# Optimization experiments

Measured on AMD Instinct MI355X. Metric: run time of the kernel, lower is better.

The kernel has to match this reference:

```python
import jax, jax.numpy as jnp
from jax import lax
import numpy as np

# (in_ch, out_ch, kernel) per SparseConv layer; last layer has no ReLU
LAYERS = [(1, 16, 11), (16, 16, 7), (16, 16, 5), (16, 16, 3), (16, 16, 3), (16, 1, 1)]
DN = ('NCHW', 'OIHW', 'NCHW')


def _sparse_conv(x, mask, w, bias, gamma, beta, relu):
    k = w.shape[-1]
    p = k // 2
    pad = [(p, p), (p, p)]
    xm = x * mask  # mask broadcasts over channels ([B,1,H,W])
    y = lax.conv_general_dilated(xm, w, (1, 1), pad, dimension_numbers=DN)
    # 'sparsity' conv: fixed all-ones [1,1,k,k] kernel over the 1-channel mask
    ones_k = jnp.ones((1, 1, k, k), x.dtype)
    s = lax.conv_general_dilated(mask, ones_k, (1, 1), pad, dimension_numbers=DN)
    y = y * (1.0 / (s + 1e-8)) + bias[None, :, None, None]
    # BatchNorm2d in training mode (batch statistics), eps=1e-5
    mean = jnp.mean(y, axis=(0, 2, 3), keepdims=True)
    var = jnp.var(y, axis=(0, 2, 3), keepdims=True)
    y = (y - mean) * lax.rsqrt(var + 1e-5)
    y = y * gamma[None, :, None, None] + beta[None, :, None, None]
    if relu:
        y = jnp.maximum(y, 0.0)
    # MaxPool2d(k, stride=1, padding=k//2) on the mask (pads with -inf)
    mask = lax.reduce_window(mask, -jnp.inf, lax.max, (1, 1, k, k), (1, 1, 1, 1),
                             [(0, 0), (0, 0), (p, p), (p, p)])
    return y, mask


def setup_inputs() -> dict:
    key = jax.random.key(0)
    kx, *kws = jax.random.split(key, 1 + len(LAYERS))
    inp = {"x": jax.random.uniform(kx, (4, 2, 1024, 1024), dtype=jnp.float32)}
    for i, (cin, cout, k) in enumerate(LAYERS, start=1):
        fan_in = cin * k * k
        inp[f"w{i}"] = jax.random.normal(kws[i - 1], (cout, cin, k, k), jnp.float32) / np.sqrt(fan_in)
        inp[f"b{i}"] = jnp.zeros((cout,), jnp.float32)
        inp[f"g{i}"] = jnp.ones((cout,), jnp.float32)
        inp[f"bt{i}"] = jnp.zeros((cout,), jnp.float32)
    return inp


def reference(x, w1, b1, g1, bt1, w2, b2, g2, bt2, w3, b3, g3, bt3,
              w4, b4, g4, bt4, w5, b5, g5, bt5, w6, b6, g6, bt6):
    data = x[:, 0:1]   # channels != 1 (input_channels=2 -> channel 0)
    mask = x[:, 1:2]   # channel 1
    params = [(w1, b1, g1, bt1), (w2, b2, g2, bt2), (w3, b3, g3, bt3),
              (w4, b4, g4, bt4), (w5, b5, g5, bt5), (w6, b6, g6, bt6)]
    h, m = data, mask
    for i, (w, b, g, bt) in enumerate(params):
        h, m = _sparse_conv(h, m, w, b, g, bt, relu=(i < 5))
    return h
```

## Files before the change

kernel.cpp:

```cpp
#include <hip/hip_runtime.h>
#include <hip/hip_bf16.h>


#define HW (1024 * 1024)
typedef __hip_bfloat16 bf16;
typedef __attribute__((ext_vector_type(8))) short s8v;
typedef __attribute__((ext_vector_type(4))) float f4v;

__device__ __forceinline__ float b2f(bf16 v) { return __bfloat162float(v); }
__device__ __forceinline__ bf16  f2b(float v) { return __float2bfloat16(v); }
__device__ __forceinline__ short fbits(float v) {
    bf16 t = f2b(v); short s; __builtin_memcpy(&s, &t, 2); return s;
}
__device__ __forceinline__ float bs2f(short s) {
    bf16 t; __builtin_memcpy(&t, &s, 2); return __bfloat162float(t);
}

__device__ __forceinline__ float ldv(const void* p, int i, bool isf) {
    return isf ? ((const float*)p)[i] : b2f(((const bf16*)p)[i]);
}

__device__ __forceinline__ float wave_reduce(float v) {
    #pragma unroll
    for (int off = 32; off > 0; off >>= 1)
        v += __shfl_down(v, off, 64);
    return v;
}

__global__ void probeKernel(const unsigned short* __restrict__ xb,
                            float* __restrict__ stats)
{
    __shared__ int sbad;
    const int tid = threadIdx.x;
    if (tid == 0) sbad = 0;
    __syncthreads();
    int bad = 0;
    for (int i = tid; i < 4096; i += 256) {
        unsigned u = ((unsigned)xb[i]) << 16;
        float v = __uint_as_float(u);
        if (!(v >= 0.f && v < 1.f)) bad = 1;
    }
    if (bad) sbad = 1;
    __syncthreads();
    if (tid == 0) stats[380] = sbad ? 1.f : 0.f;
}

__global__ void transposeW1(const void* __restrict__ w, bf16* __restrict__ wb,
                            const float* flagp)
{
    const bool isf = (*flagp > 0.5f);
    int j = blockIdx.x * 256 + threadIdx.x;
    if (j < 3072) {
        int col8 = j & 7;
        int co = (j >> 3) & 15;
        int k8 = j >> 7;
        int k = k8 * 8 + col8;
        int dy = k >> 4, dx = k & 15;
        float v = (dy < 11 && dx < 11) ? ldv(w, co * 121 + dy * 11 + dx, isf) : 0.f;
        wb[j] = f2b(v);
    }
}

__global__ void transposeWB(const void* __restrict__ w, bf16* __restrict__ wtB,
                            int K, int DXP, const float* flagp)
{
    const bool isf = (*flagp > 0.5f);
    int NT = K * DXP;
    int j = blockIdx.x * 256 + threadIdx.x;
    if (j < NT * 256) {
        int t = j >> 8, co = (j >> 4) & 15, c = j & 15;
        int dy = t / DXP, dx = t % DXP;
        float v = (dx < K) ? ldv(w, (co * 16 + c) * (K * K) + dy * K + dx, isf) : 0.f;
        wtB[j] = f2b(v);
    }
}

template <int TM, int TK, int WP, int BS>
__device__ __forceinline__ void buildMaskTile(
    const void* __restrict__ mask0, bool isf, float* sm0, float* vm,
    float* mprev, int bx, int by, int tid)
{
    constexpr int H1 = (TM - 32) / 2;
    constexpr int H2 = (TK - 32) / 2;
    for (int i = tid; i < TM * TM; i += BS) {
        int yy = by - H1 + i / TM, xx = bx - H1 + i % TM;
        float m = 0.f;
        if ((unsigned)yy < 1024u && (unsigned)xx < 1024u)
            m = ldv(mask0, (yy << 10) + xx, isf);
        sm0[i] = m;
    }
    __syncthreads();
    for (int i = tid; i < TK * TM; i += BS) {
        int y = i / TM, xc = i % TM;
        float mx = 0.f;
        for (int d = 0; d < WP; ++d) mx = fmaxf(mx, sm0[(y + d) * TM + xc]);
        vm[i] = mx;
    }
    __syncthreads();
    for (int i = tid; i < TK * TK; i += BS) {
        int y = i / TK, xc = i % TK;
        int gy = by - H2 + y, gx = bx - H2 + xc;
        float mx = 0.f;
        if ((unsigned)gy < 1024u && (unsigned)gx < 1024u)
            for (int d = 0; d < WP; ++d) mx = fmaxf(mx, vm[y * TM + xc + d]);
        mprev[i] = mx;
    }
    __syncthreads();
}

__device__ __forceinline__ const void* maskChanPtr(const void* x, int n, bool isf) {
    return isf ? (const void*)((const float*)x + n * 2 * HW + HW)
               : (const void*)((const bf16*)x + n * 2 * HW + HW);
}

__global__ __launch_bounds__(256) void convFirstM(
    const void* __restrict__ x, const bf16* __restrict__ wb1,
    const void* __restrict__ bias, bf16* __restrict__ out,
    float* statsCur, const float* flagp)
{
    constexpr int ST = 48, ROWS = 44, MT = 42;
    __shared__ alignas(16) short c0[ROWS * ST];
    __shared__ alignas(16) short c1[ROWS * ST + 2];
    __shared__ float smask[MT * MT];
    __shared__ float scs[32 * MT];
    __shared__ float sinv[1024];
    __shared__ float red[128];
    const bool isf = (*flagp > 0.5f);
    const int n = blockIdx.z;
    const int bx = blockIdx.x * 32, by = blockIdx.y * 32;
    const int tid = threadIdx.x, lane = tid & 63, wid = tid >> 6;
    const int nn = lane & 15, q = lane >> 4;

    s8v Bf[6];
    #pragma unroll
    for (int kb = 0; kb < 6; ++kb)
        Bf[kb] = *(const s8v*)(wb1 + ((kb * 4 + q) * 16 + nn) * 8);
    const float bv = ldv(bias, nn, isf);

    if (tid == 0) c1[0] = 0;

    const int xoff = n * 2 * HW;
    for (int i = tid; i < ROWS * ST; i += 256) {
        int row = i / ST, col = i - row * ST;
        int yy = by - 5 + row, xx = bx - 5 + col;
        float d = 0.f, m = 0.f;
        if ((unsigned)yy < 1024u && (unsigned)xx < 1024u) {
            d = ldv(x, xoff + (yy << 10) + xx, isf);
            m = ldv(x, xoff + HW + (yy << 10) + xx, isf);
        }
        short b = fbits(d * m);
        c0[i] = b;
        c1[i + 1] = b;
        if (row < MT && col < MT) smask[row * MT + col] = m;
    }
    __syncthreads();

    for (int i = tid; i < 32 * MT; i += 256) {
        int r = i / MT, c = i - r * MT;
        float s = 0.f;
        #pragma unroll
        for (int dy = 0; dy < 11; ++dy) s += smask[(r + dy) * MT + c];
        scs[i] = s;
    }
    __syncthreads();
    for (int i = tid; i < 1024; i += 256) {
        int r = i >> 5, xc = i & 31;
        float s = 0.f;
        #pragma unroll
        for (int dx = 0; dx < 11; ++dx) s += scs[r * MT + xc + dx];
        sinv[i] = 121.f / (s + 1e-8f);
    }
    __syncthreads();

    const int dyq = q >> 1, dxq = (q & 1) << 3;
    const size_t nbase = (size_t)n * HW;
    float lsum = 0.f, lsq = 0.f;

    for (int mt = 0; mt < 16; ++mt) {
        int idx = wid * 16 + mt;
        int r = idx >> 1, g = idx & 1;
        int e = (r + dyq) * ST + (g << 4) + dxq + nn;
        int s = e & 1;
        const unsigned* cp = s ? (const unsigned*)c1 : (const unsigned*)c0;
        int w = (e + s) >> 1;
        f4v acc0 = {0.f, 0.f, 0.f, 0.f}, acc1 = {0.f, 0.f, 0.f, 0.f};
        #pragma unroll
        for (int kb = 0; kb < 6; ++kb) {
            union { unsigned u[4]; s8v v; } A;
            A.u[0] = cp[w];
            A.u[1] = cp[w + 1];
            A.u[2] = cp[w + 2];
            A.u[3] = cp[w + 3];
            if (kb & 1)
                acc1 = __builtin_amdgcn_mfma_f32_16x16x32_bf16(A.v, Bf[kb], acc1, 0, 0, 0);
            else
                acc0 = __builtin_amdgcn_mfma_f32_16x16x32_bf16(A.v, Bf[kb], acc0, 0, 0, 0);
            w += ST;
        }
        #pragma unroll
        for (int i2 = 0; i2 < 4; ++i2) {
            int px = (g << 4) + (q << 2) + i2;
            float y = fmaf(acc0[i2] + acc1[i2], sinv[(r << 5) + px], bv);
            out[((nbase + ((by + r) << 10) + bx + px) << 4) + nn] = f2b(y);
            lsum += y;
            lsq = fmaf(y, y, lsq);
        }
    }

    lsum += __shfl_xor(lsum, 16, 64);
    lsum += __shfl_xor(lsum, 32, 64);
    lsq  += __shfl_xor(lsq, 16, 64);
    lsq  += __shfl_xor(lsq, 32, 64);
    if (lane < 16) {
        red[wid * 32 + lane]      = lsum;
        red[wid * 32 + 16 + lane] = lsq;
    }
    __syncthreads();
    if (tid < 32) {
        float t = red[tid] + red[32 + tid] + red[64 + tid] + red[96 + tid];
        atomicAdd(&statsCur[tid], t);
    }
}

template <int K, int WP, int DXP, int JG>
__global__ __launch_bounds__(512, 4) void conv16m(
    const bf16* __restrict__ in, const void* __restrict__ x,
    const bf16* __restrict__ wtB, const float* statsPrev,
    const void* __restrict__ bias, bf16* __restrict__ out,
    float* statsCur, const float* flagp)
{
    constexpr int TK = 32 + K - 1;
    constexpr int TM = TK + WP - 1;
    constexpr int NJ = DXP / 2;
    constexpr int NJG = NJ / JG;
    static_assert(NJ % JG == 0, "NJ must be divisible by JG");
    constexpr int KK = K * K;
    constexpr int H2 = K / 2;
    __shared__ short sdatL[(TK * TK + 1) * 8];
    __shared__ short sdatH[(TK * TK + 1) * 8];
    __shared__ float mprev[TK * TK];
    __shared__ float sinv[1024];
    __shared__ float red[256];
    __shared__ float sss[32];
    const bool isf = (*flagp > 0.5f);
    const int n = blockIdx.z;
    const int bx = blockIdx.x * 32, by = blockIdx.y * 32;
    const int tid = threadIdx.x, lane = tid & 63, wid = tid >> 6;

    if (tid < 16) { sss[tid] = statsPrev[32 + tid]; sss[16 + tid] = statsPrev[48 + tid]; }

    buildMaskTile<TM, TK, WP, 512>(maskChanPtr(x, n, isf), isf,
                                   (float*)sdatL, (float*)sdatH, mprev, bx, by, tid);

    {
        float* cs = (float*)sdatH;
        for (int i = tid; i < 32 * TK; i += 512) {
            int r = i / TK, c = i - r * TK;
            float s = 0.f;
            #pragma unroll
            for (int dy = 0; dy < K; ++dy) s += mprev[(r + dy) * TK + c];
            cs[i] = s;
        }
        __syncthreads();
        for (int i = tid; i < 1024; i += 512) {
            int r = i >> 5, xc = i & 31;
            float s = 0.f;
            #pragma unroll
            for (int dx = 0; dx < K; ++dx) s += cs[r * TK + xc + dx];
            sinv[i] = (float)KK / (s + 1e-8f);
        }
        __syncthreads();
    }

    const int nn = lane & 15, quad = lane >> 4, c0 = (quad & 1) * 8, tl = quad >> 1;

    {
        const bf16* inb = in + ((size_t)n * HW << 4);
        for (int p = tid; p < TK * TK; p += 512) {
            int yy = by - H2 + p / TK, xx = bx - H2 + p % TK;
            s8v lo = {0,0,0,0,0,0,0,0}, hi = {0,0,0,0,0,0,0,0};
            if ((unsigned)yy < 1024u && (unsigned)xx < 1024u) {
                float mv = mprev[p];
                const s8v* q = (const s8v*)(inb + ((size_t)((yy << 10) + xx) << 4));
                s8v rl = q[0], rh = q[1];
                #pragma unroll
                for (int c = 0; c < 8; ++c) {
                    float yv = bs2f(rl[c]);
                    lo[c] = fbits(fmaxf(fmaf(sss[c], yv, sss[16 + c]), 0.f) * mv);
                }
                #pragma unroll
                for (int c = 0; c < 8; ++c) {
                    float yv = bs2f(rh[c]);
                    hi[c] = fbits(fmaxf(fmaf(sss[c + 8], yv, sss[24 + c]), 0.f) * mv);
                }
            }
            ((s8v*)sdatL)[p] = lo;
            ((s8v*)sdatH)[p] = hi;
        }
        if (tid == 0) {
            s8v z = {0,0,0,0,0,0,0,0};
            ((s8v*)sdatL)[TK * TK] = z;
            ((s8v*)sdatH)[TK * TK] = z;
        }
    }
    __syncthreads();

    const float bv = ldv(bias, nn, isf);
    const s8v* Abase = (const s8v*)((quad & 1) ? sdatH : sdatL);
    const size_t nbase = (size_t)n * HW;
    const int r0 = wid * 4;

    f4v acc[4][2];
    #pragma unroll
    for (int rr = 0; rr < 4; ++rr) {
        acc[rr][0] = f4v{0.f, 0.f, 0.f, 0.f};
        acc[rr][1] = f4v{0.f, 0.f, 0.f, 0.f};
    }

    #pragma unroll
    for (int jg = 0; jg < NJG; ++jg) {
        s8v Bf[K * JG];
        #pragma unroll
        for (int kk = 0; kk < K * JG; ++kk) {
            int dy = kk / JG, jj = kk % JG;
            int t = dy * DXP + 2 * (jg * JG + jj) + tl;
            Bf[kk] = *(const s8v*)(wtB + ((t * 16 + nn) * 16 + c0));
        }
        #pragma unroll
        for (int ar = 0; ar < 4 + K - 1; ++ar) {
            #pragma unroll
            for (int jj = 0; jj < JG; ++jj) {
                const int j = jg * JG + jj;
                const int base = (r0 + ar) * TK + nn + 2 * j + tl;
                const s8v F0 = Abase[base];
                const s8v F1 = Abase[base + 16];
                #pragma unroll
                for (int dy = 0; dy < K; ++dy) {
                    if (ar - dy >= 0 && ar - dy < 4) {
                        acc[ar - dy][0] = __builtin_amdgcn_mfma_f32_16x16x32_bf16(
                            F0, Bf[dy * JG + jj], acc[ar - dy][0], 0, 0, 0);
                        acc[ar - dy][1] = __builtin_amdgcn_mfma_f32_16x16x32_bf16(
                            F1, Bf[dy * JG + jj], acc[ar - dy][1], 0, 0, 0);
                    }
                }
            }
        }
    }

    float lsum = 0.f, lsq = 0.f;
    #pragma unroll
    for (int rr = 0; rr < 4; ++rr) {
        const int r = r0 + rr;
        #pragma unroll
        for (int h = 0; h < 2; ++h) {
            const int xh = h << 4;
            #pragma unroll
            for (int i = 0; i < 4; ++i) {
                int m = quad * 4 + i;
                float y = fmaf(acc[rr][h][i], sinv[r * 32 + xh + m], bv);
                out[((nbase + ((by + r) << 10) + bx + xh + m) << 4) + nn] = f2b(y);
                lsum += y;
                lsq = fmaf(y, y, lsq);
            }
        }
    }

    lsum += __shfl_xor(lsum, 16, 64);
    lsum += __shfl_xor(lsum, 32, 64);
    lsq  += __shfl_xor(lsq, 16, 64);
    lsq  += __shfl_xor(lsq, 32, 64);
    if (lane < 16) {
        red[wid * 32 + lane]      = lsum;
        red[wid * 32 + 16 + lane] = lsq;
    }
    __syncthreads();
    if (tid < 32) {
        float t = 0.f;
        #pragma unroll
        for (int w8 = 0; w8 < 8; ++w8) t += red[w8 * 32 + tid];
        atomicAdd(&statsCur[tid], t);
    }
}

__global__ __launch_bounds__(256) void layer6Kernel(
    const bf16* __restrict__ in, const void* __restrict__ x,
    const float* statsPrev, const void* __restrict__ w6,
    const void* __restrict__ b6, bf16* __restrict__ y6,
    float* statsCur, const float* flagp)
{
    constexpr int WP = 25, TM = 56, TK = 32;
    __shared__ float sm0[TM * TM];
    __shared__ float vm[TK * TM];
    __shared__ float m5[TK * TK];
    __shared__ float red[8];
    __shared__ float ssc[16], ssh[16];
    const bool isf = (*flagp > 0.5f);
    const int n = blockIdx.z;
    const int bx = blockIdx.x * 32, by = blockIdx.y * 32;
    const int tid = threadIdx.x;
    const int tx = tid & 31, ty0 = (tid >> 5) << 2;

    if (tid < 16) {
        ssc[tid] = statsPrev[32 + tid];
        ssh[tid] = statsPrev[48 + tid];
    }

    buildMaskTile<TM, TK, WP, 256>(maskChanPtr(x, n, isf), isf, sm0, vm, m5, bx, by, tid);

    float wv[16];
    #pragma unroll
    for (int c = 0; c < 16; ++c) wv[c] = ldv(w6, c, isf);
    const float bias = ldv(b6, 0, isf);

    float lsum = 0.f, lsq = 0.f;
    #pragma unroll
    for (int p = 0; p < 4; ++p) {
        int yy = by + ty0 + p, xx = bx + tx;
        float m = m5[(ty0 + p) * TK + tx];
        const s8v* q = (const s8v*)(in + (((size_t)n * HW + (yy << 10) + xx) << 4));
        s8v rl = q[0], rh = q[1];
        float a = 0.f;
        #pragma unroll
        for (int c = 0; c < 8; ++c) {
            float h = fmaxf(fmaf(ssc[c], bs2f(rl[c]), ssh[c]), 0.f);
            a = fmaf(h, wv[c], a);
        }
        #pragma unroll
        for (int c = 0; c < 8; ++c) {
            float h = fmaxf(fmaf(ssc[c + 8], bs2f(rh[c]), ssh[c + 8]), 0.f);
            a = fmaf(h, wv[c + 8], a);
        }
        float yv = a * m / (m + 1e-8f) + bias;
        y6[n * HW + (yy << 10) + xx] = f2b(yv);
        lsum += yv;
        lsq = fmaf(yv, yv, lsq);
    }
    lsum = wave_reduce(lsum);
    lsq = wave_reduce(lsq);
    const int wid = tid >> 6, lane = tid & 63;
    if (lane == 0) { red[wid] = lsum; red[4 + wid] = lsq; }
    __syncthreads();
    if (tid == 0) atomicAdd(&statsCur[0],  red[0] + red[1] + red[2] + red[3]);
    if (tid == 1) atomicAdd(&statsCur[16], red[4] + red[5] + red[6] + red[7]);
}

__global__ void finalizeStats(float* stats, const void* __restrict__ g,
                              const void* __restrict__ bt, float alpha, int cout,
                              float* mirror, const float* flagp)
{
    const bool isf = (*flagp > 0.5f);
    int c = threadIdx.x;
    if (c < cout) {
        const float invN = 1.f / (4.f * HW);
        float meanp = stats[c] * invN;
        float varp  = fmaxf(stats[16 + c] * invN - meanp * meanp, 0.f);
        float var_t = varp / (alpha * alpha);
        float sct = ldv(g, c, isf) * rsqrtf(var_t + 1e-5f);
        float scp = sct / alpha;
        float shp = ldv(bt, c, isf) - scp * meanp;
        stats[32 + c] = scp;
        stats[48 + c] = shp;
        if (mirror) { mirror[2 * c] = scp; mirror[2 * c + 1] = shp; mirror[32] = isf ? 1.f : 0.f; }
    }
}

__global__ void finalOut(const bf16* __restrict__ y6, const float* mirror,
                         void* __restrict__ out)
{
    float sc = mirror[0], sh = mirror[1];
    const bool isf = (mirror[32] > 0.5f);
    for (int idx = blockIdx.x * 256 + threadIdx.x; idx < 4 * HW; idx += gridDim.x * 256) {
        float v = fmaf(b2f(y6[idx]), sc, sh);
        if (isf) ((float*)out)[idx] = v;
        else     ((bf16*)out)[idx] = f2b(v);
    }
}

__global__ void zeroStats(float* stats)
{
    int i = blockIdx.x * 256 + threadIdx.x;
    if (i < 384) stats[i] = 0.f;
}

__global__ void fillOut(void* out, const float* flagp, float v)
{
    const bool isf = (*flagp > 0.5f);
    for (int idx = blockIdx.x * 256 + threadIdx.x; idx < 4 * HW; idx += gridDim.x * 256) {
        if (isf) ((float*)out)[idx] = v;
        else     ((bf16*)out)[idx] = f2b(v);
    }
}

extern "C" void kernel_launch(void* const* d_in, const int* in_sizes, int n_in,
                              void* d_out, int out_size, void* d_ws, size_t ws_size,
                              hipStream_t stream)
{
    const void* x = d_in[0];
    #define W(L)  ((const void*)d_in[1 + ((L) - 1) * 4])
    #define B(L)  ((const void*)d_in[2 + ((L) - 1) * 4])
    #define G(L)  ((const void*)d_in[3 + ((L) - 1) * 4])
    #define BT(L) ((const void*)d_in[4 + ((L) - 1) * 4])

    float* stats = (float*)d_out;
    const float* flagp = stats + 380;
    float* wt1 = stats + 384;
    bf16* wb1 = (bf16*)wt1;
    bf16* wb2 = (bf16*)(wt1 + 1936);
    bf16* wb3 = wb2 + 56 * 256;
    bf16* wb4 = wb3 + 30 * 256;
    bf16* wb5 = wb4 + 12 * 256;
    const size_t need = 2 * (size_t)64 * HW * sizeof(bf16);

    zeroStats<<<2, 256, 0, stream>>>(stats);
    probeKernel<<<1, 256, 0, stream>>>((const unsigned short*)x, stats);

    if (ws_size < need) {
        fillOut<<<2048, 256, 0, stream>>>(d_out, flagp, 3.0f);
        return;
    }

    transposeW1<<<12, 256, 0, stream>>>(W(1), wb1, flagp);
    transposeWB<<<56, 256, 0, stream>>>(W(2), wb2, 7, 8, flagp);
    transposeWB<<<30, 256, 0, stream>>>(W(3), wb3, 5, 6, flagp);
    transposeWB<<<12, 256, 0, stream>>>(W(4), wb4, 3, 4, flagp);
    transposeWB<<<12, 256, 0, stream>>>(W(5), wb5, 3, 4, flagp);

    bf16* bufA = (bf16*)d_ws;
    bf16* bufB = bufA + 64 * HW;
    float* mirror = (float*)bufA;

    dim3 grid(32, 32, 4), block(256), block5(512);

    convFirstM<<<grid, block, 0, stream>>>(x, wb1, B(1), bufA, stats + 0, flagp);
    finalizeStats<<<1, 64, 0, stream>>>(stats + 0, G(1), BT(1), 121.f, 16, nullptr, flagp);

    conv16m<7, 11, 8, 2><<<grid, block5, 0, stream>>>(bufA, x, wb2, stats + 0, B(2), bufB, stats + 64, flagp);
    finalizeStats<<<1, 64, 0, stream>>>(stats + 64, G(2), BT(2), 49.f, 16, nullptr, flagp);

    conv16m<5, 17, 6, 3><<<grid, block5, 0, stream>>>(bufB, x, wb3, stats + 64, B(3), bufA, stats + 128, flagp);
    finalizeStats<<<1, 64, 0, stream>>>(stats + 128, G(3), BT(3), 25.f, 16, nullptr, flagp);

    conv16m<3, 21, 4, 2><<<grid, block5, 0, stream>>>(bufA, x, wb4, stats + 128, B(4), bufB, stats + 192, flagp);
    finalizeStats<<<1, 64, 0, stream>>>(stats + 192, G(4), BT(4), 9.f, 16, nullptr, flagp);

    conv16m<3, 23, 4, 2><<<grid, block5, 0, stream>>>(bufB, x, wb5, stats + 192, B(5), bufA, stats + 256, flagp);
    finalizeStats<<<1, 64, 0, stream>>>(stats + 256, G(5), BT(5), 9.f, 16, nullptr, flagp);

    bf16* y6 = (bf16*)bufB;
    layer6Kernel<<<grid, block, 0, stream>>>(bufA, x, stats + 256, W(6), B(6), y6, stats + 320, flagp);
    finalizeStats<<<1, 64, 0, stream>>>(stats + 320, G(6), BT(6), 1.f, 1, mirror, flagp);
    finalOut<<<2048, 256, 0, stream>>>(y6, mirror, d_out);

    #undef W
    #undef B
    #undef G
    #undef BT
}
```

Baseline: 727.4 us.

## Cascade dilated masks through global bf16 buffers instead of recomputing from input

Each layer now writes its max-pooled mask to a global bf16 buffer, and the next layer reads it, replacing the large-window cumulative max-pool rebuild from the raw input mask. Mask window sums and maxes are fused in one pass. This removes the growing WP-wide halo reads and max reductions in layers 2 to 6. In exchange it adds an extra 4M-element mask write and read per layer, needs more workspace, and falls back to the old path when the workspace is too small. It also stores the mask in bf16, which is exact only if mask values are binary; the test input is uniform floats, so results may differ.

```diff
diff --git a/kernel.cpp b/kernel.cpp
--- a/kernel.cpp
+++ b/kernel.cpp
@@ -116,7 +116,7 @@
 __global__ __launch_bounds__(256) void convFirstM(
     const void* __restrict__ x, const bf16* __restrict__ wb1,
     const void* __restrict__ bias, bf16* __restrict__ out,
-    float* statsCur, const float* flagp)
+    float* statsCur, const float* flagp, bf16* __restrict__ mOut)
 {
     constexpr int ST = 48, ROWS = 44, MT = 42;
     __shared__ alignas(16) short c0[ROWS * ST];
@@ -172,6 +172,25 @@
     }
     __syncthreads();
 
+    if (mOut != nullptr) {
+        for (int i = tid; i < 32 * MT; i += 256) {
+            int r = i / MT, c = i - r * MT;
+            float mx = 0.f;
+            #pragma unroll
+            for (int dy = 0; dy < 11; ++dy) mx = fmaxf(mx, smask[(r + dy) * MT + c]);
+            scs[i] = mx;
+        }
+        __syncthreads();
+        bf16* mo = mOut + (size_t)n * HW;
+        for (int i = tid; i < 1024; i += 256) {
+            int r = i >> 5, xc = i & 31;
+            float mx = 0.f;
+            #pragma unroll
+            for (int dx = 0; dx < 11; ++dx) mx = fmaxf(mx, scs[r * MT + xc + dx]);
+            mo[((by + r) << 10) + bx + xc] = f2b(mx);
+        }
+    }
+
     const int dyq = q >> 1, dxq = (q & 1) << 3;
     const size_t nbase = (size_t)n * HW;
     float lsum = 0.f, lsq = 0.f;
@@ -222,12 +241,13 @@
     }
 }
 
-template <int K, int WP, int DXP, int JG>
+template <int K, int WP, int DXP, int JG, bool CAS>
 __global__ __launch_bounds__(512, 4) void conv16m(
     const bf16* __restrict__ in, const void* __restrict__ x,
     const bf16* __restrict__ wtB, const float* statsPrev,
     const void* __restrict__ bias, bf16* __restrict__ out,
-    float* statsCur, const float* flagp)
+    float* statsCur, const float* flagp,
+    const bf16* __restrict__ mIn, bf16* __restrict__ mOut)
 {
     constexpr int TK = 32 + K - 1;
     constexpr int TM = TK + WP - 1;
@@ -249,10 +269,47 @@
 
     if (tid < 16) { sss[tid] = statsPrev[32 + tid]; sss[16 + tid] = statsPrev[48 + tid]; }
 
-    buildMaskTile<TM, TK, WP, 512>(maskChanPtr(x, n, isf), isf,
-                                   (float*)sdatL, (float*)sdatH, mprev, bx, by, tid);
-
-    {
+    if constexpr (CAS) {
+        const bf16* mp = mIn + (size_t)n * HW;
+        for (int i = tid; i < TK * TK; i += 512) {
+            int yy = by - H2 + i / TK, xx = bx - H2 + i % TK;
+            float m = 0.f;
+            if ((unsigned)yy < 1024u && (unsigned)xx < 1024u)
+                m = b2f(mp[(yy << 10) + xx]);
+            mprev[i] = m;
+        }
+        __syncthreads();
+        float* cs = (float*)sdatH;
+        float* cm = (float*)sdatL;
+        for (int i = tid; i < 32 * TK; i += 512) {
+            int r = i / TK, c = i - r * TK;
+            float s = 0.f, mx = 0.f;
+            #pragma unroll
+            for (int dy = 0; dy < K; ++dy) {
+                float v = mprev[(r + dy) * TK + c];
+                s += v;
+                mx = fmaxf(mx, v);
+            }
+            cs[i] = s;
+            cm[i] = mx;
+        }
+        __syncthreads();
+        bf16* mo = mOut + (size_t)n * HW;
+        for (int i = tid; i < 1024; i += 512) {
+            int r = i >> 5, xc = i & 31;
+            float s = 0.f, mx = 0.f;
+            #pragma unroll
+            for (int dx = 0; dx < K; ++dx) {
+                s += cs[r * TK + xc + dx];
+                mx = fmaxf(mx, cm[r * TK + xc + dx]);
+            }
+            sinv[i] = (float)KK / (s + 1e-8f);
+            mo[((by + r) << 10) + bx + xc] = f2b(mx);
+        }
+        __syncthreads();
+    } else {
+        buildMaskTile<TM, TK, WP, 512>(maskChanPtr(x, n, isf), isf,
+                                       (float*)sdatL, (float*)sdatH, mprev, bx, by, tid);
         float* cs = (float*)sdatH;
         for (int i = tid; i < 32 * TK; i += 512) {
             int r = i / TK, c = i - r * TK;
@@ -382,16 +439,17 @@
     }
 }
 
+template <bool CAS>
 __global__ __launch_bounds__(256) void layer6Kernel(
     const bf16* __restrict__ in, const void* __restrict__ x,
     const float* statsPrev, const void* __restrict__ w6,
     const void* __restrict__ b6, bf16* __restrict__ y6,
-    float* statsCur, const float* flagp)
+    float* statsCur, const float* flagp, const bf16* __restrict__ mIn)
 {
     constexpr int WP = 25, TM = 56, TK = 32;
-    __shared__ float sm0[TM * TM];
-    __shared__ float vm[TK * TM];
-    __shared__ float m5[TK * TK];
+    __shared__ float sm0[CAS ? 1 : TM * TM];
+    __shared__ float vm[CAS ? 1 : TK * TM];
+    __shared__ float m5[CAS ? 1 : TK * TK];
     __shared__ float red[8];
     __shared__ float ssc[16], ssh[16];
     const bool isf = (*flagp > 0.5f);
@@ -405,7 +463,11 @@
         ssh[tid] = statsPrev[48 + tid];
     }
 
-    buildMaskTile<TM, TK, WP, 256>(maskChanPtr(x, n, isf), isf, sm0, vm, m5, bx, by, tid);
+    if constexpr (!CAS) {
+        buildMaskTile<TM, TK, WP, 256>(maskChanPtr(x, n, isf), isf, sm0, vm, m5, bx, by, tid);
+    } else {
+        __syncthreads();
+    }
 
     float wv[16];
     #pragma unroll
@@ -416,7 +478,9 @@
     #pragma unroll
     for (int p = 0; p < 4; ++p) {
         int yy = by + ty0 + p, xx = bx + tx;
-        float m = m5[(ty0 + p) * TK + tx];
+        float m;
+        if constexpr (CAS) m = b2f(mIn[(size_t)n * HW + (yy << 10) + xx]);
+        else               m = m5[(ty0 + p) * TK + tx];
         const s8v* q = (const s8v*)(in + (((size_t)n * HW + (yy << 10) + xx) << 4));
         s8v rl = q[0], rh = q[1];
         float a = 0.f;
@@ -510,6 +574,7 @@
     bf16* wb4 = wb3 + 30 * 256;
     bf16* wb5 = wb4 + 12 * 256;
     const size_t need = 2 * (size_t)64 * HW * sizeof(bf16);
+    const size_t need2 = need + (size_t)16 * HW;
 
     zeroStats<<<2, 256, 0, stream>>>(stats);
     probeKernel<<<1, 256, 0, stream>>>((const unsigned short*)x, stats);
@@ -526,30 +591,53 @@
     transposeWB<<<12, 256, 0, stream>>>(W(5), wb5, 3, 4, flagp);
 
     bf16* bufA = (bf16*)d_ws;
-    bf16* bufB = bufA + 64 * HW;
+    bf16* bufB = bufA + 64 * (size_t)HW;
+    bf16* mA   = bufB + 64 * (size_t)HW;
+    bf16* mB   = mA + 4 * (size_t)HW;
     float* mirror = (float*)bufA;
+    const bool roomy = (ws_size >= need2);
 
     dim3 grid(32, 32, 4), block(256), block5(512);
 
-    convFirstM<<<grid, block, 0, stream>>>(x, wb1, B(1), bufA, stats + 0, flagp);
+    convFirstM<<<grid, block, 0, stream>>>(x, wb1, B(1), bufA, stats + 0, flagp,
+                                           roomy ? mA : nullptr);
     finalizeStats<<<1, 64, 0, stream>>>(stats + 0, G(1), BT(1), 121.f, 16, nullptr, flagp);
 
-    conv16m<7, 11, 8, 2><<<grid, block5, 0, stream>>>(bufA, x, wb2, stats + 0, B(2), bufB, stats + 64, flagp);
-    finalizeStats<<<1, 64, 0, stream>>>(stats + 64, G(2), BT(2), 49.f, 16, nullptr, flagp);
-
-    conv16m<5, 17, 6, 3><<<grid, block5, 0, stream>>>(bufB, x, wb3, stats + 64, B(3), bufA, stats + 128, flagp);
-    finalizeStats<<<1, 64, 0, stream>>>(stats + 128, G(3), BT(3), 25.f, 16, nullptr, flagp);
-
-    conv16m<3, 21, 4, 2><<<grid, block5, 0, stream>>>(bufA, x, wb4, stats + 128, B(4), bufB, stats + 192, flagp);
-    finalizeStats<<<1, 64, 0, stream>>>(stats + 192, G(4), BT(4), 9.f, 16, nullptr, flagp);
-
-    conv16m<3, 23, 4, 2><<<grid, block5, 0, stream>>>(bufB, x, wb5, stats + 192, B(5), bufA, stats + 256, flagp);
-    finalizeStats<<<1, 64, 0, stream>>>(stats + 256, G(5), BT(5), 9.f, 16, nullptr, flagp);
-
-    bf16* y6 = (bf16*)bufB;
-    layer6Kernel<<<grid, block, 0, stream>>>(bufA, x, stats + 256, W(6), B(6), y6, stats + 320, flagp);
-    finalizeStats<<<1, 64, 0, stream>>>(stats + 320, G(6), BT(6), 1.f, 1, mirror, flagp);
-    finalOut<<<2048, 256, 0, stream>>>(y6, mirror, d_out);
+    if (roomy) {
+        conv16m<7, 11, 8, 2, true><<<grid, block5, 0, stream>>>(bufA, x, wb2, stats + 0, B(2), bufB, stats + 64, flagp, mA, mB);
+        finalizeStats<<<1, 64, 0, stream>>>(stats + 64, G(2), BT(2), 49.f, 16, nullptr, flagp);
+
+        conv16m<5, 17, 6, 3, true><<<grid, block5, 0, stream>>>(bufB, x, wb3, stats + 64, B(3), bufA, stats + 128, flagp, mB, mA);
+        finalizeStats<<<1, 64, 0, stream>>>(stats + 128, G(3), BT(3), 25.f, 16, nullptr, flagp);
+
+        conv16m<3, 21, 4, 2, true><<<grid, block5, 0, stream>>>(bufA, x, wb4, stats + 128, B(4), bufB, stats + 192, flagp, mA, mB);
+        finalizeStats<<<1, 64, 0, stream>>>(stats + 192, G(4), BT(4), 9.f, 16, nullptr, flagp);
+
+        conv16m<3, 23, 4, 2, true><<<grid, block5, 0, stream>>>(bufB, x, wb5, stats + 192, B(5), bufA, stats + 256, flagp, mB, mA);
+        finalizeStats<<<1, 64, 0, stream>>>(stats + 256, G(5), BT(5), 9.f, 16, nullptr, flagp);
+
+        bf16* y6 = (bf16*)bufB;
+        layer6Kernel<true><<<grid, block, 0, stream>>>(bufA, x, stats + 256, W(6), B(6), y6, stats + 320, flagp, mA);
+        finalizeStats<<<1, 64, 0, stream>>>(stats + 320, G(6), BT(6), 1.f, 1, mirror, flagp);
+        finalOut<<<2048, 256, 0, stream>>>(y6, mirror, d_out);
+    } else {
+        conv16m<7, 11, 8, 2, false><<<grid, block5, 0, stream>>>(bufA, x, wb2, stats + 0, B(2), bufB, stats + 64, flagp, nullptr, nullptr);
+        finalizeStats<<<1, 64, 0, stream>>>(stats + 64, G(2), BT(2), 49.f, 16, nullptr, flagp);
+
+        conv16m<5, 17, 6, 3, false><<<grid, block5, 0, stream>>>(bufB, x, wb3, stats + 64, B(3), bufA, stats + 128, flagp, nullptr, nullptr);
+        finalizeStats<<<1, 64, 0, stream>>>(stats + 128, G(3), BT(3), 25.f, 16, nullptr, flagp);
+
+        conv16m<3, 21, 4, 2, false><<<grid, block5, 0, stream>>>(bufA, x, wb4, stats + 128, B(4), bufB, stats + 192, flagp, nullptr, nullptr);
+        finalizeStats<<<1, 64, 0, stream>>>(stats + 192, G(4), BT(4), 9.f, 16, nullptr, flagp);
+
+        conv16m<3, 23, 4, 2, false><<<grid, block5, 0, stream>>>(bufB, x, wb5, stats + 192, B(5), bufA, stats + 256, flagp, nullptr, nullptr);
+        finalizeStats<<<1, 64, 0, stream>>>(stats + 256, G(5), BT(5), 9.f, 16, nullptr, flagp);
+
+        bf16* y6 = (bf16*)bufB;
+        layer6Kernel<false><<<grid, block, 0, stream>>>(bufA, x, stats + 256, W(6), B(6), y6, stats + 320, flagp, nullptr);
+        finalizeStats<<<1, 64, 0, stream>>>(stats + 320, G(6), BT(6), 1.f, 1, mirror, flagp);
+        finalOut<<<2048, 256, 0, stream>>>(y6, mirror, d_out);
+    }
 
     #undef W
     #undef B
```

Result: no change. 719.8 us (-1.0%).
